# Kernel tuning notes

Hardware: AMD Instinct MI355X
Metric: run time of the kernel (lower is better)

## Reference

```python
import jax, jax.numpy as jnp
import numpy as np

N = 100000   # nodes
E = 600000   # edges
F = 128      # node_feat
HID = 128    # hidden
H = 4        # heads
D = HID // H # head dim
NT = 3       # node types
ET = 4       # edge types
SLOPE = 0.2  # leaky relu slope for attention logits


def hetero_linear(x, types, W, b):
    # per-type linear: out[n] = x[n] @ W[types[n]] + b[types[n]]
    # one-hot contraction avoids gathering a full [N,in,out] weight tensor
    T = W.shape[0]
    oh = jax.nn.one_hot(types, T, dtype=x.dtype)
    return jnp.einsum('ni,nt,tio->no', x, oh, W) + b[types]


def setup_inputs() -> dict:
    key = jax.random.key(0)
    ks = jax.random.split(key, 20)
    f32 = jnp.float32
    s_in = 1.0 / np.sqrt(F)
    s_h = 1.0 / np.sqrt(HID)
    inp = {
        'x': jax.random.normal(ks[0], (N, F), f32),
        'edge_index': jax.random.randint(ks[1], (2, E), 0, N),
        'node_type': jax.random.randint(ks[2], (N,), 0, NT),
        'edge_type': jax.random.randint(ks[3], (E,), 0, ET),
        'edge_attr': jax.random.normal(ks[4], (E, 1), f32),
        # EHATConv params: per-node-type q/k/v projections
        'Wq': jax.random.normal(ks[5], (NT, F, HID), f32) * s_in,
        'Wk': jax.random.normal(ks[6], (NT, F, HID), f32) * s_in,
        'Wv': jax.random.normal(ks[7], (NT, F, HID), f32) * s_in,
        # per-head attention vectors
        'att_src': jax.random.normal(ks[8], (H, D), f32) * s_h,
        'att_dst': jax.random.normal(ks[9], (H, D), f32) * s_h,
        'att_edge': jax.random.normal(ks[10], (H, D), f32) * s_h,
        # per-edge-type edge-attr embedding (edge_dim=1 -> hidden)
        'We': jax.random.normal(ks[11], (ET, 1, HID), f32),
        'be': jax.random.normal(ks[12], (ET, HID), f32) * s_h,
        # HeteroLinear classifiers
        'Wn': jax.random.normal(ks[13], (NT, HID, 1), f32) * s_h,
        'bn': jnp.zeros((NT, 1), f32),
        'Wec': jax.random.normal(ks[14], (ET, HID, 1), f32) * s_h,
        'bec': jnp.zeros((ET, 1), f32),
    }
    return inp


def reference(x, edge_index, node_type, edge_type, edge_attr,
              Wq, Wk, Wv, att_src, att_dst, att_edge, We, be, Wn, bn, Wec, bec):
    src, dst = edge_index[0], edge_index[1]
    n = x.shape[0]
    e = edge_type.shape[0]

    # forward passes zeros as edge_attr into the conv (as in original module)
    eattr = jnp.zeros((e, 1), x.dtype)

    # per-node-type q/k/v projections -> [N,H,D]
    q = hetero_linear(x, node_type, Wq, jnp.zeros((NT, HID), x.dtype)).reshape(n, H, D)
    k = hetero_linear(x, node_type, Wk, jnp.zeros((NT, HID), x.dtype)).reshape(n, H, D)
    v = hetero_linear(x, node_type, Wv, jnp.zeros((NT, HID), x.dtype)).reshape(n, H, D)

    # per-edge-type edge-attr embedding -> [E,H,D]
    e_emb = (jnp.einsum('ni,nio->no', eattr, We[edge_type]) + be[edge_type]).reshape(e, H, D)

    # attention logits per edge/head
    logits = (jnp.einsum('ehd,hd->eh', k[src], att_src)
              + jnp.einsum('ehd,hd->eh', q[dst], att_dst)
              + jnp.einsum('ehd,hd->eh', e_emb, att_edge))
    logits = jnp.where(logits >= 0, logits, SLOPE * logits)

    # segment softmax over incoming edges of each destination node
    m = jax.ops.segment_max(logits, dst, num_segments=n)  # [N,H]
    p = jnp.exp(logits - m[dst])
    denom = jax.ops.segment_sum(p, dst, num_segments=n)   # [N,H]
    alpha = p / (denom[dst] + 1e-16)                       # [E,H]

    # messages and aggregation
    msg = (v[src] + e_emb) * alpha[:, :, None]             # [E,H,D]
    e_out = msg.reshape(e, HID)
    x_out = jax.ops.segment_sum(e_out, dst, num_segments=n)  # [N,HID]

    # nonlin (relu; dropout identity in eval)
    x_h = jax.nn.relu(x_out)
    e_h = jax.nn.relu(e_out)

    # hetero classifiers
    x_cls = hetero_linear(x_h, node_type, Wn, bn)   # [N,1]
    e_cls = hetero_linear(e_h, edge_type, Wec, bec) # [E,1]
    return (x_cls, e_cls)
```

## Files before the change

kernel.cpp:

```cpp
#include <hip/hip_runtime.h>
#include <hip/hip_bf16.h>


#define NN 100000
#define NE 600000
#define FD 128
#define HIDD 128
#define NH 4
#define DH 32
#define NT 3
#define NET 4
#define SLOPE 0.2f
#define CAP 32
#define NBLK_EDGE 2344
#define NBLK_PRE  33

typedef short bf16x8 __attribute__((ext_vector_type(8)));
typedef float f32x4 __attribute__((ext_vector_type(4)));

#define OFF_V       0UL
#define OFF_KS      25600000UL
#define OFF_QD      27200000UL
#define OFF_R       28800000UL
#define OFF_COUNTS  35200000UL
#define OFF_EDGES   35600128UL
#define OFF_ETL     61200128UL
#define OFF_WPACK   61200256UL
#define OFF_BEP     61396864UL
#define OFF_WECP    61398912UL
#define OFF_WNP     61400960UL
#define OFF_WKQP    61402496UL

__device__ __forceinline__ unsigned int pack_bf16(float a, float b) {
    __hip_bfloat16 ha = __float2bfloat16(a);
    __hip_bfloat16 hb = __float2bfloat16(b);
    unsigned short ua = *reinterpret_cast<unsigned short*>(&ha);
    unsigned short ub = *reinterpret_cast<unsigned short*>(&hb);
    return (unsigned int)ua | ((unsigned int)ub << 16);
}

union U8 { uint4 u; bf16x8 v; };

__global__ void k_build(const int* __restrict__ ei, const int* __restrict__ etype,
                        int* __restrict__ counts, uint2* __restrict__ edges,
                        const float* __restrict__ Wq, const float* __restrict__ Wk,
                        const float* __restrict__ Wv,
                        const float* __restrict__ att_src, const float* __restrict__ att_dst,
                        const float* __restrict__ be, const float* __restrict__ att_edge,
                        const float* __restrict__ Wec, const float* __restrict__ Wn,
                        float* __restrict__ etl, unsigned int* __restrict__ wpack,
                        float* __restrict__ bep, float* __restrict__ wecp,
                        float* __restrict__ wnp, unsigned int* __restrict__ wkqp) {
    if (blockIdx.x >= NBLK_EDGE) {
        int pgid = (blockIdx.x - NBLK_EDGE) * 256 + threadIdx.x;
        if (pgid < 16) {
            int t = pgid >> 2, h = pgid & 3;
            float s = 0.f;
            for (int d = 0; d < DH; ++d) s += be[t * HIDD + h * DH + d] * att_edge[h * DH + d];
            etl[t * NH + h] = s;
        } else if (pgid >= 64 && pgid < 64 + NT * 8 * 4 * 64) {
            int q = pgid - 64;
            int t = q >> 11;
            int rem = q & 2047;
            int ot = rem >> 8;
            int rem2 = rem & 255;
            int kc = rem2 >> 6;
            int l = rem2 & 63;
            int o = ot * 16 + (l & 15);
            int kb = kc * 32 + (l >> 4) * 8;
            unsigned int w[4];
#pragma unroll
            for (int jj = 0; jj < 4; ++jj) {
                float v0 = Wv[((size_t)t * FD + kb + 2 * jj) * HIDD + o];
                float v1 = Wv[((size_t)t * FD + kb + 2 * jj + 1) * HIDD + o];
                w[jj] = pack_bf16(v0, v1);
            }
            uint4 o4 = {w[0], w[1], w[2], w[3]};
            *reinterpret_cast<uint4*>(wpack + (size_t)q * 4) = o4;
        } else if (pgid >= 6208 && pgid < 7616) {
            int p = pgid - 6208;
            int dp = p & 127;
            int col = dp >> 3, ot = dp & 7;
            int od = ot * 16 + col;
            if (p < 512) {
                int t2 = p >> 7;
                bep[p] = be[t2 * HIDD + od];
            } else if (p < 1024) {
                int t2 = (p - 512) >> 7;
                wecp[p - 512] = Wec[t2 * HIDD + od];
            } else {
                int t = (p - 1024) >> 7;
                wnp[p - 1024] = Wn[t * HIDD + od];
            }
        } else if (pgid >= 7616 && pgid < 7616 + NT * 4 * 64) {
            int q2 = pgid - 7616;
            int t = q2 >> 8;
            int rem = q2 & 255;
            int kc = rem >> 6;
            int l = rem & 63;
            int col = l & 15, kg = l >> 4;
            unsigned int w[4];
#pragma unroll
            for (int jj = 0; jj < 4; ++jj) {
                float v01[2];
#pragma unroll
                for (int sub = 0; sub < 2; ++sub) {
                    int k = kc * 32 + kg * 8 + 2 * jj + sub;
                    float s = 0.f;
                    if (col < 4) {
                        const float* wrow = Wk + ((size_t)t * FD + k) * HIDD + col * DH;
                        const float* arow = att_src + col * DH;
                        for (int d = 0; d < DH; ++d) s += wrow[d] * arow[d];
                    } else if (col < 8) {
                        int h = col - 4;
                        const float* wrow = Wq + ((size_t)t * FD + k) * HIDD + h * DH;
                        const float* arow = att_dst + h * DH;
                        for (int d = 0; d < DH; ++d) s += wrow[d] * arow[d];
                    }
                    v01[sub] = s;
                }
                w[jj] = pack_bf16(v01[0], v01[1]);
            }
            uint4 o4 = {w[0], w[1], w[2], w[3]};
            *reinterpret_cast<uint4*>(wkqp + (size_t)q2 * 4) = o4;
        }
        return;
    }
    int i = blockIdx.x * blockDim.x + threadIdx.x;
    if (i < NE) {
        int dst = ei[NE + i];
        int pos = atomicAdd(&counts[dst], 1);
        if (pos < CAP) {
            uint2 rec;
            rec.x = ((unsigned)ei[i] << 2) | (unsigned)etype[i];
            rec.y = (unsigned)i;
            edges[(size_t)dst * CAP + pos] = rec;
        }
    }
}

__global__ __launch_bounds__(256) void k_node(const float* __restrict__ x,
                                              const unsigned short* __restrict__ wpack,
                                              const unsigned short* __restrict__ wkqp,
                                              const int* __restrict__ ntype,
                                              const float* __restrict__ bep, const float* __restrict__ wecp,
                                              unsigned short* __restrict__ vb, float* __restrict__ ks4,
                                              float* __restrict__ qd4, float* __restrict__ rtab) {
    int wave = threadIdx.x >> 6, lane = threadIdx.x & 63;
    int base = blockIdx.x * 64 + wave * 16;
    if (base >= NN) return;
    int col = lane & 15, kg = lane >> 4;
    int n = base + col;
    int tcol = (n < NN) ? ntype[n] : -1;
    int an = n < NN ? n : NN - 1;

    const float* xp = x + (size_t)an * FD;
    bf16x8 afrag[4];
#pragma unroll
    for (int kc = 0; kc < 4; ++kc) {
        float4 a4 = *reinterpret_cast<const float4*>(xp + kc * 32 + kg * 8);
        float4 b4 = *reinterpret_cast<const float4*>(xp + kc * 32 + kg * 8 + 4);
        U8 u;
        u.u.x = pack_bf16(a4.x, a4.y);
        u.u.y = pack_bf16(a4.z, a4.w);
        u.u.z = pack_bf16(b4.x, b4.y);
        u.u.w = pack_bf16(b4.z, b4.w);
        afrag[kc] = u.v;
    }

    int dn[4], tdn[4];
#pragma unroll
    for (int rg = 0; rg < 4; ++rg) {
        dn[rg] = base + kg * 4 + rg;
        tdn[rg] = __shfl(tcol, kg * 4 + rg, 64);
    }

    f32x4 res[8];
#pragma unroll
    for (int ot = 0; ot < 8; ++ot) { f32x4 z = {0.f, 0.f, 0.f, 0.f}; res[ot] = z; }
    f32x4 rkq = {0.f, 0.f, 0.f, 0.f};

    for (int t = 0; t < NT; ++t) {
        if (__ballot(tcol == t) == 0ull) continue;
        bf16x8 am[4];
#pragma unroll
        for (int kc = 0; kc < 4; ++kc) {
            U8 z; z.u.x = z.u.y = z.u.z = z.u.w = 0u;
            am[kc] = (tcol == t) ? afrag[kc] : z.v;
        }
        const unsigned short* wt = wpack + (size_t)t * 8 * 4 * 64 * 8;
        const unsigned short* wq = wkqp + (size_t)t * 4 * 64 * 8;
        f32x4 acc[8];
#pragma unroll
        for (int ot = 0; ot < 8; ++ot) { f32x4 z = {0.f, 0.f, 0.f, 0.f}; acc[ot] = z; }
        f32x4 akq = {0.f, 0.f, 0.f, 0.f};
#pragma unroll
        for (int kc = 0; kc < 4; ++kc) {
            bf16x8 bq = *reinterpret_cast<const bf16x8*>(wq + ((size_t)kc * 64 + lane) * 8);
            akq = __builtin_amdgcn_mfma_f32_16x16x32_bf16(am[kc], bq, akq, 0, 0, 0);
#pragma unroll
            for (int ot = 0; ot < 8; ++ot) {
                bf16x8 b = *reinterpret_cast<const bf16x8*>(wt + ((size_t)(ot * 4 + kc) * 64 + lane) * 8);
                acc[ot] = __builtin_amdgcn_mfma_f32_16x16x32_bf16(am[kc], b, acc[ot], 0, 0, 0);
            }
        }
#pragma unroll
        for (int rg = 0; rg < 4; ++rg) {
            bool mine = (tdn[rg] == t);
#pragma unroll
            for (int ot = 0; ot < 8; ++ot) res[ot][rg] = mine ? acc[ot][rg] : res[ot][rg];
            rkq[rg] = mine ? akq[rg] : rkq[rg];
        }
    }

    if (col < 8) {
        float* dst = (col < 4) ? ks4 : qd4;
        int h = col & 3;
#pragma unroll
        for (int rg = 0; rg < 4; ++rg)
            if (dn[rg] < NN) dst[(size_t)dn[rg] * NH + h] = rkq[rg];
    }

#pragma unroll
    for (int rg = 0; rg < 4; ++rg) {
        if (dn[rg] < NN) {
            uint4 o4;
            o4.x = pack_bf16(res[0][rg], res[1][rg]);
            o4.y = pack_bf16(res[2][rg], res[3][rg]);
            o4.z = pack_bf16(res[4][rg], res[5][rg]);
            o4.w = pack_bf16(res[6][rg], res[7][rg]);
            *reinterpret_cast<uint4*>(vb + (size_t)dn[rg] * FD + col * 8) = o4;
        }
    }

#pragma unroll
    for (int rg = 0; rg < 4; ++rg) {
        float cur[16];
#pragma unroll
        for (int t2 = 0; t2 < NET; ++t2) {
            float4 b0 = *reinterpret_cast<const float4*>(bep + t2 * HIDD + col * 8);
            float4 b1 = *reinterpret_cast<const float4*>(bep + t2 * HIDD + col * 8 + 4);
            float4 w0 = *reinterpret_cast<const float4*>(wecp + t2 * HIDD + col * 8);
            float4 w1 = *reinterpret_cast<const float4*>(wecp + t2 * HIDD + col * 8 + 4);
            cur[t2 * 4 + 0] = fmaxf(res[0][rg] + b0.x, 0.f) * w0.x + fmaxf(res[1][rg] + b0.y, 0.f) * w0.y;
            cur[t2 * 4 + 1] = fmaxf(res[2][rg] + b0.z, 0.f) * w0.z + fmaxf(res[3][rg] + b0.w, 0.f) * w0.w;
            cur[t2 * 4 + 2] = fmaxf(res[4][rg] + b1.x, 0.f) * w1.x + fmaxf(res[5][rg] + b1.y, 0.f) * w1.y;
            cur[t2 * 4 + 3] = fmaxf(res[6][rg] + b1.z, 0.f) * w1.z + fmaxf(res[7][rg] + b1.w, 0.f) * w1.w;
        }
        int cb = col & 1;
        float n8[8];
#pragma unroll
        for (int i = 0; i < 8; ++i) {
            float keep = cb ? cur[2 * i + 1] : cur[2 * i];
            float give = cb ? cur[2 * i] : cur[2 * i + 1];
            n8[i] = keep + __shfl_xor(give, 1, 64);
        }
        cb = (col >> 1) & 1;
        float n4[4];
#pragma unroll
        for (int i = 0; i < 4; ++i) {
            float keep = cb ? n8[2 * i + 1] : n8[2 * i];
            float give = cb ? n8[2 * i] : n8[2 * i + 1];
            n4[i] = keep + __shfl_xor(give, 2, 64);
        }
        cb = (col >> 2) & 1;
        float n2[2];
#pragma unroll
        for (int i = 0; i < 2; ++i) {
            float keep = cb ? n4[2 * i + 1] : n4[2 * i];
            float give = cb ? n4[2 * i] : n4[2 * i + 1];
            n2[i] = keep + __shfl_xor(give, 4, 64);
        }
        cb = (col >> 3) & 1;
        {
            float keep = cb ? n2[1] : n2[0];
            float give = cb ? n2[0] : n2[1];
            float tot = keep + __shfl_xor(give, 8, 64);
            if (dn[rg] < NN) rtab[(size_t)dn[rg] * 16 + col] = tot;
        }
    }
}

__global__ __launch_bounds__(256) void k_main(const int* __restrict__ counts, const uint2* __restrict__ edges,
                                              const float* __restrict__ ks4, const float* __restrict__ qd4,
                                              const float* __restrict__ etl, const unsigned int* __restrict__ vb,
                                              const float* __restrict__ bep, const float* __restrict__ rtab,
                                              const float* __restrict__ bec, const float* __restrict__ wnp,
                                              const float* __restrict__ bn, const int* __restrict__ ntype,
                                              float* __restrict__ out_x, float* __restrict__ out_e) {
    int wave = threadIdx.x >> 6;
    int lane = threadIdx.x & 63;
    int n = blockIdx.x * 4 + wave;
    if (n >= NN) return;
    int dg = counts[n];
    dg = dg < CAP ? dg : CAP;
    int deg = __builtin_amdgcn_readfirstlane(dg);
    size_t rs = (size_t)n * CAP;
    int hh = lane & 3;
    int k0 = lane >> 2;

    float q = qd4[(size_t)n * NH + hh];

    bool act0 = k0 < deg;
    uint2 ed0 = {0u, 0u};
    if (act0) ed0 = edges[rs + k0];
    int s0r = (int)(ed0.x >> 2), et0 = (int)(ed0.x & 3u);
    float e0 = 0.f;
    if (act0) {
        float l = ks4[(size_t)s0r * NH + hh] + q + etl[et0 * NH + hh];
        l = l >= 0.f ? l : SLOPE * l;
        e0 = __expf(l);
    }
    float dn = e0;
    if (deg > 16) {
        for (int bb = 16; bb < deg; bb += 16) {
            int kk = bb + k0;
            if (kk < deg) {
                uint2 ed = edges[rs + kk];
                int s = (int)(ed.x >> 2), et = (int)(ed.x & 3u);
                float l = ks4[(size_t)s * NH + hh] + q + etl[et * NH + hh];
                l = l >= 0.f ? l : SLOPE * l;
                dn += __expf(l);
            }
        }
    }
#pragma unroll
    for (int off = 4; off < 64; off <<= 1) dn += __shfl_xor(dn, off, 64);
    float inv = 1.0f / (dn + 1e-16f);

    if (act0) {
        float term = e0 * inv * rtab[((size_t)s0r * NET + et0) * NH + hh];
        term += __shfl_xor(term, 1, 64);
        term += __shfl_xor(term, 2, 64);
        if (hh == 0) out_e[ed0.y] = term + bec[et0];
    }
    if (deg > 16) {
        for (int bb = 16; bb < deg; bb += 16) {
            int kk = bb + k0;
            if (kk < deg) {
                uint2 ed = edges[rs + kk];
                int s = (int)(ed.x >> 2), et = (int)(ed.x & 3u);
                float l = ks4[(size_t)s * NH + hh] + q + etl[et * NH + hh];
                l = l >= 0.f ? l : SLOPE * l;
                float term = __expf(l) * inv * rtab[((size_t)s * NET + et) * NH + hh];
                term += __shfl_xor(term, 1, 64);
                term += __shfl_xor(term, 2, 64);
                if (hh == 0) out_e[ed.y] = term + bec[et];
            }
        }
    }

    float2 beL0 = *reinterpret_cast<const float2*>(bep + 0 * HIDD + 2 * lane);
    float2 beL1 = *reinterpret_cast<const float2*>(bep + 1 * HIDD + 2 * lane);
    float2 beL2 = *reinterpret_cast<const float2*>(bep + 2 * HIDD + 2 * lane);
    float2 beL3 = *reinterpret_cast<const float2*>(bep + 3 * HIDD + 2 * lane);
    float alpha0 = e0 * inv;
    float ax = 0.f, ay = 0.f;
    int c0 = deg < 16 ? deg : 16;
#define AGGH(J) { \
        uint2 er = edges[rs + (J)]; \
        int sn = (int)(er.x >> 2); int et = (int)(er.x & 3u); \
        unsigned int w = vb[(size_t)sn * 64 + lane]; \
        float a = __shfl(alpha0, 4 * (J) + hh, 64); \
        float2 b2 = et == 0 ? beL0 : et == 1 ? beL1 : et == 2 ? beL2 : beL3; \
        ax = fmaf(a, __uint_as_float(w << 16) + b2.x, ax); \
        ay = fmaf(a, __uint_as_float(w & 0xffff0000u) + b2.y, ay); }
    {
        int j = 0;
        for (; j + 4 <= c0; j += 4) {
            AGGH(j) AGGH(j + 1) AGGH(j + 2) AGGH(j + 3)
        }
        for (; j < c0; ++j) AGGH(j)
    }
#undef AGGH
    if (deg > 16) {
        for (int bb = 16; bb < deg; bb += 16) {
            int kk = bb + k0;
            float al = 0.f;
            if (kk < deg) {
                uint2 ed = edges[rs + kk];
                int s = (int)(ed.x >> 2), et = (int)(ed.x & 3u);
                float l = ks4[(size_t)s * NH + hh] + q + etl[et * NH + hh];
                l = l >= 0.f ? l : SLOPE * l;
                al = __expf(l) * inv;
            }
            int cnt = deg - bb; if (cnt > 16) cnt = 16;
#define AGGH2(J) { \
            uint2 er = edges[rs + bb + (J)]; \
            int sn = (int)(er.x >> 2); int et = (int)(er.x & 3u); \
            unsigned int w = vb[(size_t)sn * 64 + lane]; \
            float a = __shfl(al, 4 * (J) + hh, 64); \
            float2 b2 = et == 0 ? beL0 : et == 1 ? beL1 : et == 2 ? beL2 : beL3; \
            ax = fmaf(a, __uint_as_float(w << 16) + b2.x, ax); \
            ay = fmaf(a, __uint_as_float(w & 0xffff0000u) + b2.y, ay); }
            int j = 0;
            for (; j + 4 <= cnt; j += 4) {
                AGGH2(j) AGGH2(j + 1) AGGH2(j + 2) AGGH2(j + 3)
            }
            for (; j < cnt; ++j) AGGH2(j)
#undef AGGH2
        }
    }

    int t = ntype[n];
    float2 w2 = *reinterpret_cast<const float2*>(wnp + t * HIDD + 2 * lane);
    float s = fmaxf(ax, 0.f) * w2.x + fmaxf(ay, 0.f) * w2.y;
#pragma unroll
    for (int off = 1; off < 64; off <<= 1) s += __shfl_xor(s, off, 64);
    if (lane == 0) out_x[n] = s + bn[t];
}

extern "C" void kernel_launch(void* const* d_in, const int* in_sizes, int n_in,
                              void* d_out, int out_size, void* d_ws, size_t ws_size,
                              hipStream_t stream) {
    const float* x        = (const float*)d_in[0];
    const int*   ei       = (const int*)d_in[1];
    const int*   ntype    = (const int*)d_in[2];
    const int*   etype    = (const int*)d_in[3];
    const float* Wq       = (const float*)d_in[5];
    const float* Wk       = (const float*)d_in[6];
    const float* Wv       = (const float*)d_in[7];
    const float* att_src  = (const float*)d_in[8];
    const float* att_dst  = (const float*)d_in[9];
    const float* att_edge = (const float*)d_in[10];
    const float* be       = (const float*)d_in[12];
    const float* Wn       = (const float*)d_in[13];
    const float* bn       = (const float*)d_in[14];
    const float* Wec      = (const float*)d_in[15];
    const float* bec      = (const float*)d_in[16];

    char* ws = (char*)d_ws;
    unsigned int*   vb32 = (unsigned int*)(ws + OFF_V);
    unsigned short* vb16 = (unsigned short*)(ws + OFF_V);
    float* ks4     = (float*)(ws + OFF_KS);
    float* qd4     = (float*)(ws + OFF_QD);
    float* rtab    = (float*)(ws + OFF_R);
    int*   counts  = (int*)(ws + OFF_COUNTS);
    uint2* edges   = (uint2*)(ws + OFF_EDGES);
    float* etl     = (float*)(ws + OFF_ETL);
    unsigned int* wpack = (unsigned int*)(ws + OFF_WPACK);
    float* bep     = (float*)(ws + OFF_BEP);
    float* wecp    = (float*)(ws + OFF_WECP);
    float* wnp     = (float*)(ws + OFF_WNP);
    unsigned int* wkqp = (unsigned int*)(ws + OFF_WKQP);

    float* out_x = (float*)d_out;
    float* out_e = (float*)d_out + NN;

    hipMemsetAsync(ws + OFF_COUNTS, 0, 400000, stream);
    k_build<<<NBLK_EDGE + NBLK_PRE, 256, 0, stream>>>(ei, etype, counts, edges,
                                                      Wq, Wk, Wv, att_src, att_dst, be, att_edge,
                                                      Wec, Wn, etl, wpack, bep, wecp, wnp, wkqp);
    k_node<<<(NN + 63) / 64, 256, 0, stream>>>(x, (const unsigned short*)wpack,
                                               (const unsigned short*)wkqp, ntype,
                                               bep, wecp, vb16, ks4, qd4, rtab);
    k_main<<<(NN + 3) / 4, 256, 0, stream>>>(counts, edges, ks4, qd4, etl, vb32, bep,
                                             rtab, bec, wnp, bn, ntype, out_x, out_e);
}
```

Measured before the change: 194.2 us.

## Fold counts memset into weight-prep kernel and co-schedule edge bucketing with node projection

Clearing the counts array now happens inside a small weight-packing kernel, which replaces the separate memset. Edge bucketing by destination moves into the node-projection kernel as extra blocks. Node projection and edge scatter therefore run concurrently in one launch, removing one launch and one serialization point. The cost is a small serial pre-kernel that must finish before the combined kernel starts.

```diff
diff --git a/kernel.cpp b/kernel.cpp
--- a/kernel.cpp
+++ b/kernel.cpp
@@ -12,6 +12,7 @@
 #define NET 4
 #define SLOPE 0.2f
 #define CAP 32
+#define NBLK_NODE 1563
 #define NBLK_EDGE 2344
 #define NBLK_PRE  33
 
@@ -41,111 +42,114 @@
 
 union U8 { uint4 u; bf16x8 v; };
 
-__global__ void k_build(const int* __restrict__ ei, const int* __restrict__ etype,
-                        int* __restrict__ counts, uint2* __restrict__ edges,
-                        const float* __restrict__ Wq, const float* __restrict__ Wk,
-                        const float* __restrict__ Wv,
-                        const float* __restrict__ att_src, const float* __restrict__ att_dst,
-                        const float* __restrict__ be, const float* __restrict__ att_edge,
-                        const float* __restrict__ Wec, const float* __restrict__ Wn,
-                        float* __restrict__ etl, unsigned int* __restrict__ wpack,
-                        float* __restrict__ bep, float* __restrict__ wecp,
-                        float* __restrict__ wnp, unsigned int* __restrict__ wkqp) {
-    if (blockIdx.x >= NBLK_EDGE) {
-        int pgid = (blockIdx.x - NBLK_EDGE) * 256 + threadIdx.x;
-        if (pgid < 16) {
-            int t = pgid >> 2, h = pgid & 3;
-            float s = 0.f;
-            for (int d = 0; d < DH; ++d) s += be[t * HIDD + h * DH + d] * att_edge[h * DH + d];
-            etl[t * NH + h] = s;
-        } else if (pgid >= 64 && pgid < 64 + NT * 8 * 4 * 64) {
-            int q = pgid - 64;
-            int t = q >> 11;
-            int rem = q & 2047;
-            int ot = rem >> 8;
-            int rem2 = rem & 255;
-            int kc = rem2 >> 6;
-            int l = rem2 & 63;
-            int o = ot * 16 + (l & 15);
-            int kb = kc * 32 + (l >> 4) * 8;
-            unsigned int w[4];
-#pragma unroll
-            for (int jj = 0; jj < 4; ++jj) {
-                float v0 = Wv[((size_t)t * FD + kb + 2 * jj) * HIDD + o];
-                float v1 = Wv[((size_t)t * FD + kb + 2 * jj + 1) * HIDD + o];
-                w[jj] = pack_bf16(v0, v1);
-            }
-            uint4 o4 = {w[0], w[1], w[2], w[3]};
-            *reinterpret_cast<uint4*>(wpack + (size_t)q * 4) = o4;
-        } else if (pgid >= 6208 && pgid < 7616) {
-            int p = pgid - 6208;
-            int dp = p & 127;
-            int col = dp >> 3, ot = dp & 7;
-            int od = ot * 16 + col;
-            if (p < 512) {
-                int t2 = p >> 7;
-                bep[p] = be[t2 * HIDD + od];
-            } else if (p < 1024) {
-                int t2 = (p - 512) >> 7;
-                wecp[p - 512] = Wec[t2 * HIDD + od];
-            } else {
-                int t = (p - 1024) >> 7;
-                wnp[p - 1024] = Wn[t * HIDD + od];
-            }
-        } else if (pgid >= 7616 && pgid < 7616 + NT * 4 * 64) {
-            int q2 = pgid - 7616;
-            int t = q2 >> 8;
-            int rem = q2 & 255;
-            int kc = rem >> 6;
-            int l = rem & 63;
-            int col = l & 15, kg = l >> 4;
-            unsigned int w[4];
-#pragma unroll
-            for (int jj = 0; jj < 4; ++jj) {
-                float v01[2];
-#pragma unroll
-                for (int sub = 0; sub < 2; ++sub) {
-                    int k = kc * 32 + kg * 8 + 2 * jj + sub;
-                    float s = 0.f;
-                    if (col < 4) {
-                        const float* wrow = Wk + ((size_t)t * FD + k) * HIDD + col * DH;
-                        const float* arow = att_src + col * DH;
-                        for (int d = 0; d < DH; ++d) s += wrow[d] * arow[d];
-                    } else if (col < 8) {
-                        int h = col - 4;
-                        const float* wrow = Wq + ((size_t)t * FD + k) * HIDD + h * DH;
-                        const float* arow = att_dst + h * DH;
-                        for (int d = 0; d < DH; ++d) s += wrow[d] * arow[d];
-                    }
-                    v01[sub] = s;
+__global__ void k_pre(const float* __restrict__ Wq, const float* __restrict__ Wk,
+                      const float* __restrict__ Wv,
+                      const float* __restrict__ att_src, const float* __restrict__ att_dst,
+                      const float* __restrict__ be, const float* __restrict__ att_edge,
+                      const float* __restrict__ Wec, const float* __restrict__ Wn,
+                      int* __restrict__ counts,
+                      float* __restrict__ etl, unsigned int* __restrict__ wpack,
+                      float* __restrict__ bep, float* __restrict__ wecp,
+                      float* __restrict__ wnp, unsigned int* __restrict__ wkqp) {
+    int pgid = blockIdx.x * 256 + threadIdx.x;
+    for (int i = pgid; i < NN; i += NBLK_PRE * 256) counts[i] = 0;
+    if (pgid < 16) {
+        int t = pgid >> 2, h = pgid & 3;
+        float s = 0.f;
+        for (int d = 0; d < DH; ++d) s += be[t * HIDD + h * DH + d] * att_edge[h * DH + d];
+        etl[t * NH + h] = s;
+    } else if (pgid >= 64 && pgid < 64 + NT * 8 * 4 * 64) {
+        int q = pgid - 64;
+        int t = q >> 11;
+        int rem = q & 2047;
+        int ot = rem >> 8;
+        int rem2 = rem & 255;
+        int kc = rem2 >> 6;
+        int l = rem2 & 63;
+        int o = ot * 16 + (l & 15);
+        int kb = kc * 32 + (l >> 4) * 8;
+        unsigned int w[4];
+#pragma unroll
+        for (int jj = 0; jj < 4; ++jj) {
+            float v0 = Wv[((size_t)t * FD + kb + 2 * jj) * HIDD + o];
+            float v1 = Wv[((size_t)t * FD + kb + 2 * jj + 1) * HIDD + o];
+            w[jj] = pack_bf16(v0, v1);
+        }
+        uint4 o4 = {w[0], w[1], w[2], w[3]};
+        *reinterpret_cast<uint4*>(wpack + (size_t)q * 4) = o4;
+    } else if (pgid >= 6208 && pgid < 7616) {
+        int p = pgid - 6208;
+        int dp = p & 127;
+        int col = dp >> 3, ot = dp & 7;
+        int od = ot * 16 + col;
+        if (p < 512) {
+            int t2 = p >> 7;
+            bep[p] = be[t2 * HIDD + od];
+        } else if (p < 1024) {
+            int t2 = (p - 512) >> 7;
+            wecp[p - 512] = Wec[t2 * HIDD + od];
+        } else {
+            int t = (p - 1024) >> 7;
+            wnp[p - 1024] = Wn[t * HIDD + od];
+        }
+    } else if (pgid >= 7616 && pgid < 7616 + NT * 4 * 64) {
+        int q2 = pgid - 7616;
+        int t = q2 >> 8;
+        int rem = q2 & 255;
+        int kc = rem >> 6;
+        int l = rem & 63;
+        int col = l & 15, kg = l >> 4;
+        unsigned int w[4];
+#pragma unroll
+        for (int jj = 0; jj < 4; ++jj) {
+            float v01[2];
+#pragma unroll
+            for (int sub = 0; sub < 2; ++sub) {
+                int k = kc * 32 + kg * 8 + 2 * jj + sub;
+                float s = 0.f;
+                if (col < 4) {
+                    const float* wrow = Wk + ((size_t)t * FD + k) * HIDD + col * DH;
+                    const float* arow = att_src + col * DH;
+                    for (int d = 0; d < DH; ++d) s += wrow[d] * arow[d];
+                } else if (col < 8) {
+                    int h = col - 4;
+                    const float* wrow = Wq + ((size_t)t * FD + k) * HIDD + h * DH;
+                    const float* arow = att_dst + h * DH;
+                    for (int d = 0; d < DH; ++d) s += wrow[d] * arow[d];
                 }
-                w[jj] = pack_bf16(v01[0], v01[1]);
-            }
-            uint4 o4 = {w[0], w[1], w[2], w[3]};
-            *reinterpret_cast<uint4*>(wkqp + (size_t)q2 * 4) = o4;
+                v01[sub] = s;
+            }
+            w[jj] = pack_bf16(v01[0], v01[1]);
+        }
+        uint4 o4 = {w[0], w[1], w[2], w[3]};
+        *reinterpret_cast<uint4*>(wkqp + (size_t)q2 * 4) = o4;
+    }
+}
+
+__global__ __launch_bounds__(256) void k_worker(const float* __restrict__ x,
+                                                const unsigned short* __restrict__ wpack,
+                                                const unsigned short* __restrict__ wkqp,
+                                                const int* __restrict__ ntype,
+                                                const float* __restrict__ bep, const float* __restrict__ wecp,
+                                                unsigned short* __restrict__ vb, float* __restrict__ ks4,
+                                                float* __restrict__ qd4, float* __restrict__ rtab,
+                                                const int* __restrict__ ei, const int* __restrict__ etype,
+                                                int* __restrict__ counts, uint2* __restrict__ edges) {
+    if (blockIdx.x >= NBLK_NODE) {
+        int i = (blockIdx.x - NBLK_NODE) * 256 + threadIdx.x;
+        if (i < NE) {
+            int dst = ei[NE + i];
+            int pos = atomicAdd(&counts[dst], 1);
+            if (pos < CAP) {
+                uint2 rec;
+                rec.x = ((unsigned)ei[i] << 2) | (unsigned)etype[i];
+                rec.y = (unsigned)i;
+                edges[(size_t)dst * CAP + pos] = rec;
+            }
         }
         return;
     }
-    int i = blockIdx.x * blockDim.x + threadIdx.x;
-    if (i < NE) {
-        int dst = ei[NE + i];
-        int pos = atomicAdd(&counts[dst], 1);
-        if (pos < CAP) {
-            uint2 rec;
-            rec.x = ((unsigned)ei[i] << 2) | (unsigned)etype[i];
-            rec.y = (unsigned)i;
-            edges[(size_t)dst * CAP + pos] = rec;
-        }
-    }
-}
-
-__global__ __launch_bounds__(256) void k_node(const float* __restrict__ x,
-                                              const unsigned short* __restrict__ wpack,
-                                              const unsigned short* __restrict__ wkqp,
-                                              const int* __restrict__ ntype,
-                                              const float* __restrict__ bep, const float* __restrict__ wecp,
-                                              unsigned short* __restrict__ vb, float* __restrict__ ks4,
-                                              float* __restrict__ qd4, float* __restrict__ rtab) {
+
     int wave = threadIdx.x >> 6, lane = threadIdx.x & 63;
     int base = blockIdx.x * 64 + wave * 16;
     if (base >= NN) return;
@@ -447,13 +451,12 @@
     float* out_x = (float*)d_out;
     float* out_e = (float*)d_out + NN;
 
-    hipMemsetAsync(ws + OFF_COUNTS, 0, 400000, stream);
-    k_build<<<NBLK_EDGE + NBLK_PRE, 256, 0, stream>>>(ei, etype, counts, edges,
-                                                      Wq, Wk, Wv, att_src, att_dst, be, att_edge,
-                                                      Wec, Wn, etl, wpack, bep, wecp, wnp, wkqp);
-    k_node<<<(NN + 63) / 64, 256, 0, stream>>>(x, (const unsigned short*)wpack,
-                                               (const unsigned short*)wkqp, ntype,
-                                               bep, wecp, vb16, ks4, qd4, rtab);
+    k_pre<<<NBLK_PRE, 256, 0, stream>>>(Wq, Wk, Wv, att_src, att_dst, be, att_edge, Wec, Wn,
+                                        counts, etl, wpack, bep, wecp, wnp, wkqp);
+    k_worker<<<NBLK_NODE + NBLK_EDGE, 256, 0, stream>>>(x, (const unsigned short*)wpack,
+                                                        (const unsigned short*)wkqp, ntype,
+                                                        bep, wecp, vb16, ks4, qd4, rtab,
+                                                        ei, etype, counts, edges);
     k_main<<<(NN + 3) / 4, 256, 0, stream>>>(counts, edges, ks4, qd4, etl, vb32, bep,
                                              rtab, bec, wnp, bn, ntype, out_x, out_e);
 }
```

Measured after the change: 248.5 us. 1.28x slower.

## Split per-node edge-classifier table into separate kernel reading bf16 V

Applied to the files above, without the earlier changes.

The per-node, per-edge-type classifier table (rtab) is no longer computed in the node projection kernel. A new kernel computes it from the bf16 V values written to memory. This shrinks the node kernel's register use and epilogue, which may raise its occupancy. The cost is an extra launch and a re-read of V. rtab is now built from bf16-rounded V rather than fp32 accumulators, a slight precision change. Separately, the main kernel now issues the rtab load for its first edge early, alongside the logit loads, to hide its latency.

```diff
diff --git a/kernel.cpp b/kernel.cpp
--- a/kernel.cpp
+++ b/kernel.cpp
@@ -143,9 +143,8 @@
                                               const unsigned short* __restrict__ wpack,
                                               const unsigned short* __restrict__ wkqp,
                                               const int* __restrict__ ntype,
-                                              const float* __restrict__ bep, const float* __restrict__ wecp,
                                               unsigned short* __restrict__ vb, float* __restrict__ ks4,
-                                              float* __restrict__ qd4, float* __restrict__ rtab) {
+                                              float* __restrict__ qd4) {
     int wave = threadIdx.x >> 6, lane = threadIdx.x & 63;
     int base = blockIdx.x * 64 + wave * 16;
     if (base >= NN) return;
@@ -232,53 +231,62 @@
             *reinterpret_cast<uint4*>(vb + (size_t)dn[rg] * FD + col * 8) = o4;
         }
     }
-
-#pragma unroll
-    for (int rg = 0; rg < 4; ++rg) {
-        float cur[16];
-#pragma unroll
-        for (int t2 = 0; t2 < NET; ++t2) {
-            float4 b0 = *reinterpret_cast<const float4*>(bep + t2 * HIDD + col * 8);
-            float4 b1 = *reinterpret_cast<const float4*>(bep + t2 * HIDD + col * 8 + 4);
-            float4 w0 = *reinterpret_cast<const float4*>(wecp + t2 * HIDD + col * 8);
-            float4 w1 = *reinterpret_cast<const float4*>(wecp + t2 * HIDD + col * 8 + 4);
-            cur[t2 * 4 + 0] = fmaxf(res[0][rg] + b0.x, 0.f) * w0.x + fmaxf(res[1][rg] + b0.y, 0.f) * w0.y;
-            cur[t2 * 4 + 1] = fmaxf(res[2][rg] + b0.z, 0.f) * w0.z + fmaxf(res[3][rg] + b0.w, 0.f) * w0.w;
-            cur[t2 * 4 + 2] = fmaxf(res[4][rg] + b1.x, 0.f) * w1.x + fmaxf(res[5][rg] + b1.y, 0.f) * w1.y;
-            cur[t2 * 4 + 3] = fmaxf(res[6][rg] + b1.z, 0.f) * w1.z + fmaxf(res[7][rg] + b1.w, 0.f) * w1.w;
-        }
-        int cb = col & 1;
-        float n8[8];
-#pragma unroll
-        for (int i = 0; i < 8; ++i) {
-            float keep = cb ? cur[2 * i + 1] : cur[2 * i];
-            float give = cb ? cur[2 * i] : cur[2 * i + 1];
-            n8[i] = keep + __shfl_xor(give, 1, 64);
-        }
-        cb = (col >> 1) & 1;
-        float n4[4];
-#pragma unroll
-        for (int i = 0; i < 4; ++i) {
-            float keep = cb ? n8[2 * i + 1] : n8[2 * i];
-            float give = cb ? n8[2 * i] : n8[2 * i + 1];
-            n4[i] = keep + __shfl_xor(give, 2, 64);
-        }
-        cb = (col >> 2) & 1;
-        float n2[2];
-#pragma unroll
-        for (int i = 0; i < 2; ++i) {
-            float keep = cb ? n4[2 * i + 1] : n4[2 * i];
-            float give = cb ? n4[2 * i] : n4[2 * i + 1];
-            n2[i] = keep + __shfl_xor(give, 4, 64);
-        }
-        cb = (col >> 3) & 1;
-        {
-            float keep = cb ? n2[1] : n2[0];
-            float give = cb ? n2[0] : n2[1];
-            float tot = keep + __shfl_xor(give, 8, 64);
-            if (dn[rg] < NN) rtab[(size_t)dn[rg] * 16 + col] = tot;
-        }
-    }
+}
+
+__global__ __launch_bounds__(256) void k_r(const unsigned int* __restrict__ vb32,
+                                           const float* __restrict__ bep, const float* __restrict__ wecp,
+                                           float* __restrict__ rtab) {
+    int tid = threadIdx.x;
+    int n = blockIdx.x * 16 + (tid >> 4);
+    if (n >= NN) return;
+    int j = tid & 15;
+    uint4 raw = *reinterpret_cast<const uint4*>(vb32 + (size_t)n * 64 + j * 4);
+    float vv[8];
+    vv[0] = __uint_as_float(raw.x << 16); vv[1] = __uint_as_float(raw.x & 0xffff0000u);
+    vv[2] = __uint_as_float(raw.y << 16); vv[3] = __uint_as_float(raw.y & 0xffff0000u);
+    vv[4] = __uint_as_float(raw.z << 16); vv[5] = __uint_as_float(raw.z & 0xffff0000u);
+    vv[6] = __uint_as_float(raw.w << 16); vv[7] = __uint_as_float(raw.w & 0xffff0000u);
+    float cur[16];
+#pragma unroll
+    for (int t2 = 0; t2 < NET; ++t2) {
+        float4 b0 = *reinterpret_cast<const float4*>(bep + t2 * HIDD + j * 8);
+        float4 b1 = *reinterpret_cast<const float4*>(bep + t2 * HIDD + j * 8 + 4);
+        float4 w0 = *reinterpret_cast<const float4*>(wecp + t2 * HIDD + j * 8);
+        float4 w1 = *reinterpret_cast<const float4*>(wecp + t2 * HIDD + j * 8 + 4);
+        cur[t2 * 4 + 0] = fmaxf(vv[0] + b0.x, 0.f) * w0.x + fmaxf(vv[1] + b0.y, 0.f) * w0.y;
+        cur[t2 * 4 + 1] = fmaxf(vv[2] + b0.z, 0.f) * w0.z + fmaxf(vv[3] + b0.w, 0.f) * w0.w;
+        cur[t2 * 4 + 2] = fmaxf(vv[4] + b1.x, 0.f) * w1.x + fmaxf(vv[5] + b1.y, 0.f) * w1.y;
+        cur[t2 * 4 + 3] = fmaxf(vv[6] + b1.z, 0.f) * w1.z + fmaxf(vv[7] + b1.w, 0.f) * w1.w;
+    }
+    int cb = j & 1;
+    float n8[8];
+#pragma unroll
+    for (int i = 0; i < 8; ++i) {
+        float keep = cb ? cur[2 * i + 1] : cur[2 * i];
+        float give = cb ? cur[2 * i] : cur[2 * i + 1];
+        n8[i] = keep + __shfl_xor(give, 1, 64);
+    }
+    cb = (j >> 1) & 1;
+    float n4[4];
+#pragma unroll
+    for (int i = 0; i < 4; ++i) {
+        float keep = cb ? n8[2 * i + 1] : n8[2 * i];
+        float give = cb ? n8[2 * i] : n8[2 * i + 1];
+        n4[i] = keep + __shfl_xor(give, 2, 64);
+    }
+    cb = (j >> 2) & 1;
+    float n2[2];
+#pragma unroll
+    for (int i = 0; i < 2; ++i) {
+        float keep = cb ? n4[2 * i + 1] : n4[2 * i];
+        float give = cb ? n4[2 * i] : n4[2 * i + 1];
+        n2[i] = keep + __shfl_xor(give, 4, 64);
+    }
+    cb = (j >> 3) & 1;
+    float keep = cb ? n2[1] : n2[0];
+    float give = cb ? n2[0] : n2[1];
+    float tot = keep + __shfl_xor(give, 8, 64);
+    rtab[(size_t)n * 16 + j] = tot;
 }
 
 __global__ __launch_bounds__(256) void k_main(const int* __restrict__ counts, const uint2* __restrict__ edges,
@@ -305,8 +313,9 @@
     uint2 ed0 = {0u, 0u};
     if (act0) ed0 = edges[rs + k0];
     int s0r = (int)(ed0.x >> 2), et0 = (int)(ed0.x & 3u);
-    float e0 = 0.f;
+    float e0 = 0.f, rt0 = 0.f;
     if (act0) {
+        rt0 = rtab[((size_t)s0r * NET + et0) * NH + hh];
         float l = ks4[(size_t)s0r * NH + hh] + q + etl[et0 * NH + hh];
         l = l >= 0.f ? l : SLOPE * l;
         e0 = __expf(l);
@@ -329,7 +338,7 @@
     float inv = 1.0f / (dn + 1e-16f);
 
     if (act0) {
-        float term = e0 * inv * rtab[((size_t)s0r * NET + et0) * NH + hh];
+        float term = e0 * inv * rt0;
         term += __shfl_xor(term, 1, 64);
         term += __shfl_xor(term, 2, 64);
         if (hh == 0) out_e[ed0.y] = term + bec[et0];
@@ -453,7 +462,8 @@
                                                       Wec, Wn, etl, wpack, bep, wecp, wnp, wkqp);
     k_node<<<(NN + 63) / 64, 256, 0, stream>>>(x, (const unsigned short*)wpack,
                                                (const unsigned short*)wkqp, ntype,
-                                               bep, wecp, vb16, ks4, qd4, rtab);
+                                               vb16, ks4, qd4);
+    k_r<<<(NN + 15) / 16, 256, 0, stream>>>(vb32, bep, wecp, rtab);
     k_main<<<(NN + 3) / 4, 256, 0, stream>>>(counts, edges, ks4, qd4, etl, vb32, bep,
                                              rtab, bec, wnp, bn, ntype, out_x, out_e);
 }
```

New measurement: 192.0 us. No clear change (-1.1%).
